# Optimization experiments

Measured on AMD Instinct MI355X. Metric: run time of the kernel, lower is better.

The kernel has to match this reference:

```python
import jax, jax.numpy as jnp
import numpy as np

NEG = -1e9  # masked-out (non-edge) additive bias


def _attn_head(seq, bias_mat, W1, a1, b1, a2, b2, W2, bW):
    # seq: [B,N,F]; W1: [F,H]; a1,a2: [H]; W2: [H,K]
    fts = jnp.einsum('bnf,fh->bnh', seq, W1)            # Conv1D(out_sz,1,no bias)
    f1 = jnp.einsum('bnh,h->bn', fts, a1) + b1          # Conv1D(1,1)
    f2 = jnp.einsum('bnh,h->bn', fts, a2) + b2          # Conv1D(1,1)
    logits = f1[:, :, None] + f2[:, None, :]            # [B,N,N] additive attention
    coefs = jax.nn.softmax(jax.nn.leaky_relu(logits, 0.2) + bias_mat, axis=-1)
    vals = jnp.einsum('bnm,bmh->bnh', coefs, fts)       # weighted aggregation
    return jnp.einsum('bnh,hk->bnk', vals, W2) + bW     # bias_add_layer1 (Dense)


def setup_inputs() -> dict:
    B, N, F, H, NH, C = 1, 4096, 512, 64, 8, 40
    key = jax.random.key(0)
    ks = jax.random.split(key, 12)
    seq = jax.random.normal(ks[0], (B, N, F), dtype=jnp.float32)
    adj = jax.random.bernoulli(ks[1], 0.01, (B, N, N)) | jnp.eye(N, dtype=bool)[None]
    bias_mat = jnp.where(adj, 0.0, NEG).astype(jnp.float32)
    s = 0.05
    # 8 stacked first-layer heads (out_sz=H)
    W1 = jax.random.normal(ks[2], (NH, F, H), dtype=jnp.float32) * s
    a1 = jax.random.normal(ks[3], (NH, H), dtype=jnp.float32) * s
    b1 = jnp.zeros((NH,), jnp.float32)
    a2 = jax.random.normal(ks[4], (NH, H), dtype=jnp.float32) * s
    b2 = jnp.zeros((NH,), jnp.float32)
    W2 = jax.random.normal(ks[5], (NH, H, H), dtype=jnp.float32) * s
    bW = jnp.zeros((NH, H), jnp.float32)
    # single output head (out_sz=nb_classes, identity activation)
    Wo1 = jax.random.normal(ks[6], (NH * H, C), dtype=jnp.float32) * s
    ao1 = jax.random.normal(ks[7], (C,), dtype=jnp.float32) * s
    bo1 = jnp.zeros((), jnp.float32)
    ao2 = jax.random.normal(ks[8], (C,), dtype=jnp.float32) * s
    bo2 = jnp.zeros((), jnp.float32)
    Wo2 = jax.random.normal(ks[9], (C, C), dtype=jnp.float32) * s
    bo = jnp.zeros((C,), jnp.float32)
    return dict(seq=seq, bias_mat=bias_mat, W1=W1, a1=a1, b1=b1, a2=a2, b2=b2,
                W2=W2, bW=bW, Wo1=Wo1, ao1=ao1, bo1=bo1, ao2=ao2, bo2=bo2,
                Wo2=Wo2, bo=bo)


def reference(seq, bias_mat, W1, a1, b1, a2, b2, W2, bW,
              Wo1, ao1, bo1, ao2, bo2, Wo2, bo):
    # first layer: 8 heads with elu activation, vmapped over head params
    heads = jax.vmap(
        lambda w1, v1, c1, v2, c2, w2, bw: jax.nn.elu(
            _attn_head(seq, bias_mat, w1, v1, c1, v2, c2, w2, bw))
    )(W1, a1, b1, a2, b2, W2, bW)                        # [NH,B,N,H]
    NH, B, N, H = heads.shape
    h1 = jnp.moveaxis(heads, 0, 2).reshape(B, N, NH * H)  # concat along features
    # output layer: 1 head, identity activation, averaged over n_heads[-1]=1
    out = _attn_head(h1, bias_mat, Wo1, ao1, bo1, ao2, bo2, Wo2, bo)
    return out / 1.0
```

## Files before the change

kernel.cpp:

```cpp
#include <hip/hip_runtime.h>
#include <cstdint>
#include <cstddef>

#define NN 4096
#define FDIM 512
#define HDIM 64
#define NHEAD 8
#define CDIM 40
#define MAXD 256

typedef __attribute__((ext_vector_type(8))) short bf16x8;
typedef __attribute__((ext_vector_type(16))) float f32x16;

__device__ __forceinline__ float wave_max64(float v) {
  for (int o = 32; o; o >>= 1) v = fmaxf(v, __shfl_xor(v, o));
  return v;
}
__device__ __forceinline__ float wave_sum64(float v) {
  for (int o = 32; o; o >>= 1) v += __shfl_xor(v, o);
  return v;
}
__device__ __forceinline__ float readlane_f(float v, int sl) {
  return __uint_as_float((unsigned)__builtin_amdgcn_readlane((int)__float_as_uint(v), sl));
}
__device__ __forceinline__ int readlane_i(int v, int sl) {
  return __builtin_amdgcn_readlane(v, sl);
}
__device__ __forceinline__ unsigned short f2bf(float x) {
  unsigned u = __float_as_uint(x);
  return (unsigned short)((u + 0x7fffu + ((u >> 16) & 1u)) >> 16);
}
__device__ __forceinline__ float bf2f(unsigned short b) {
  return __uint_as_float(((unsigned)b) << 16);
}

__global__ __launch_bounds__(256) void k_prep(
    const float* __restrict__ seq, short* __restrict__ Ahi, short* __restrict__ Alo,
    const float* __restrict__ W1, short* __restrict__ Bhi, short* __restrict__ Blo,
    const float* __restrict__ W2, short* __restrict__ W2thi, short* __restrict__ W2tlo,
    const float* __restrict__ Wo1, short* __restrict__ Wo1thi, short* __restrict__ Wo1tlo) {
  __shared__ float T[64][65];
  int bx = blockIdx.x, tid = threadIdx.x;
  if (bx < 1024) {
    size_t off = (size_t)bx * 2048 + (size_t)tid * 8;
    float4 v0 = *(const float4*)(seq + off);
    float4 v1 = *(const float4*)(seq + off + 4);
    unsigned short h0 = f2bf(v0.x), h1 = f2bf(v0.y), h2 = f2bf(v0.z), h3 = f2bf(v0.w);
    unsigned short h4 = f2bf(v1.x), h5 = f2bf(v1.y), h6 = f2bf(v1.z), h7 = f2bf(v1.w);
    *(uint4*)(Ahi + off) = make_uint4(
        (unsigned)h0 | ((unsigned)h1 << 16), (unsigned)h2 | ((unsigned)h3 << 16),
        (unsigned)h4 | ((unsigned)h5 << 16), (unsigned)h6 | ((unsigned)h7 << 16));
    unsigned short l0 = f2bf(v0.x - bf2f(h0)), l1 = f2bf(v0.y - bf2f(h1));
    unsigned short l2 = f2bf(v0.z - bf2f(h2)), l3 = f2bf(v0.w - bf2f(h3));
    unsigned short l4 = f2bf(v1.x - bf2f(h4)), l5 = f2bf(v1.y - bf2f(h5));
    unsigned short l6 = f2bf(v1.z - bf2f(h6)), l7 = f2bf(v1.w - bf2f(h7));
    *(uint4*)(Alo + off) = make_uint4(
        (unsigned)l0 | ((unsigned)l1 << 16), (unsigned)l2 | ((unsigned)l3 << 16),
        (unsigned)l4 | ((unsigned)l5 << 16), (unsigned)l6 | ((unsigned)l7 << 16));
    return;
  }
  bx -= 1024;
  if (bx < 64) {
    int h = bx >> 3, kb = bx & 7;
    const float* src = W1 + ((size_t)h * FDIM + kb * 64) * HDIM;
#pragma unroll
    for (int q = 0; q < 4; ++q) {
      int fi = q * 256 + tid, kk = fi >> 4, n4 = fi & 15;
      float4 v = *(const float4*)(src + (size_t)kk * HDIM + n4 * 4);
      T[n4 * 4 + 0][kk] = v.x; T[n4 * 4 + 1][kk] = v.y;
      T[n4 * 4 + 2][kk] = v.z; T[n4 * 4 + 3][kk] = v.w;
    }
    __syncthreads();
#pragma unroll
    for (int q = 0; q < 4; ++q) {
      int fi = q * 256 + tid, n = fi >> 4, k4 = fi & 15;
      float a = T[n][k4 * 4], b = T[n][k4 * 4 + 1];
      float c = T[n][k4 * 4 + 2], d = T[n][k4 * 4 + 3];
      size_t o = ((size_t)h * 64 + n) * FDIM + kb * 64 + k4 * 4;
      unsigned short ha = f2bf(a), hb = f2bf(b), hc = f2bf(c), hd = f2bf(d);
      *(short4*)(Bhi + o) = make_short4((short)ha, (short)hb, (short)hc, (short)hd);
      *(short4*)(Blo + o) = make_short4((short)f2bf(a - bf2f(ha)), (short)f2bf(b - bf2f(hb)),
                                        (short)f2bf(c - bf2f(hc)), (short)f2bf(d - bf2f(hd)));
    }
    return;
  }
  bx -= 64;
  if (bx < 8) {
    int h = bx;
    const float* src = W2 + (size_t)h * HDIM * HDIM;
#pragma unroll
    for (int q = 0; q < 4; ++q) {
      int fi = q * 256 + tid, kk = fi >> 4, n4 = fi & 15;
      float4 v = *(const float4*)(src + (size_t)kk * HDIM + n4 * 4);
      T[n4 * 4 + 0][kk] = v.x; T[n4 * 4 + 1][kk] = v.y;
      T[n4 * 4 + 2][kk] = v.z; T[n4 * 4 + 3][kk] = v.w;
    }
    __syncthreads();
#pragma unroll
    for (int q = 0; q < 4; ++q) {
      int fi = q * 256 + tid, n = fi >> 4, k4 = fi & 15;
      float a = T[n][k4 * 4], b = T[n][k4 * 4 + 1];
      float c = T[n][k4 * 4 + 2], d = T[n][k4 * 4 + 3];
      size_t o = (size_t)h * 4096 + (size_t)n * 64 + k4 * 4;
      unsigned short ha = f2bf(a), hb = f2bf(b), hc = f2bf(c), hd = f2bf(d);
      *(short4*)(W2thi + o) = make_short4((short)ha, (short)hb, (short)hc, (short)hd);
      *(short4*)(W2tlo + o) = make_short4((short)f2bf(a - bf2f(ha)), (short)f2bf(b - bf2f(hb)),
                                          (short)f2bf(c - bf2f(hc)), (short)f2bf(d - bf2f(hd)));
    }
    return;
  }
  bx -= 8;
  {
#pragma unroll
    for (int q = 0; q < 16; ++q) {
      int idx = q * 256 + tid;
      int n = bx * 8 + (idx >> 9), k = idx & 511;
      float v = (n < CDIM) ? Wo1[(size_t)k * CDIM + n] : 0.f;
      unsigned short hv = f2bf(v);
      Wo1thi[(size_t)n * FDIM + k] = (short)hv;
      Wo1tlo[(size_t)n * FDIM + k] = (short)f2bf(v - bf2f(hv));
    }
  }
}

__global__ __launch_bounds__(256) void k_gemm(
    const short* __restrict__ Ahi, const short* __restrict__ Alo,
    const short* __restrict__ Bhi, const short* __restrict__ Blo,
    const float* __restrict__ a1, const float* __restrict__ b1,
    const float* __restrict__ a2, const float* __restrict__ b2,
    short* __restrict__ FTSb, float* __restrict__ F1t, float* __restrict__ F2t,
    const float* __restrict__ bias, int* __restrict__ nbr, int* __restrict__ cnt) {
  __shared__ short AH[4][64][16], AL[4][64][16];
  __shared__ short BH[4][128][16], BL[4][128][16];
  __shared__ int wtot[4];
  const int bx = blockIdx.x;
  const int tid = threadIdx.x, lane = tid & 63, w = tid >> 6;

  if (bx >= 256) {
    int row = bx - 256;
    int wv = w;
    const float4* r = (const float4*)(bias + (size_t)row * NN);
    unsigned mask = 0;
#pragma unroll
    for (int i = 0; i < 4; ++i) {
      float4 v = r[tid * 4 + i];
      mask |= (unsigned)((v.x == 0.f ? 1 : 0) | (v.y == 0.f ? 2 : 0) |
                         (v.z == 0.f ? 4 : 0) | (v.w == 0.f ? 8 : 0)) << (i * 4);
    }
    int c = __popc(mask);
    int pre = c;
#pragma unroll
    for (int o = 1; o < 64; o <<= 1) {
      int u = __shfl_up(pre, o);
      if (lane >= o) pre += u;
    }
    if (lane == 63) wtot[wv] = pre;
    __syncthreads();
    int woff = 0;
#pragma unroll
    for (int ww = 0; ww < 4; ++ww)
      if (ww < wv) woff += wtot[ww];
    int excl = woff + pre - c;
    int* outp = nbr + (size_t)row * MAXD;
    int col0 = tid * 16, k = 0;
#pragma unroll
    for (int i = 0; i < 16; ++i) {
      if ((mask >> i) & 1) {
        int p = excl + k;
        if (p < MAXD) outp[p] = col0 + i;
        ++k;
      }
    }
    if (tid == 0) {
      int total = wtot[0] + wtot[1] + wtot[2] + wtot[3];
      cnt[row] = total < MAXD ? total : MAXD;
    }
    return;
  }

  const int mtile = bx & 63, npair = bx >> 6;
  const int wm = w >> 1, wn = w & 1;
  const int ml = lane & 31, g = lane >> 5, g8 = g * 8;

  f32x16 acc0, acc1;
#pragma unroll
  for (int r = 0; r < 16; ++r) { acc0[r] = 0.f; acc1[r] = 0.f; }

  const short* Abh = Ahi + (((size_t)mtile * 64) << 9);
  const short* Abl = Alo + (((size_t)mtile * 64) << 9);
  const short* Bbh = Bhi + (((size_t)npair * 128) << 9);
  const short* Bbl = Blo + (((size_t)npair * 128) << 9);

  const int tn = tid >> 3, k8 = tid & 7;
  const int ks = k8 >> 1, ko = (k8 & 1) * 8;
  const size_t so = ((size_t)tn << 9) + (size_t)k8 * 8;

  int4 rah0, rah1, ral0, ral1, rbh0, rbh1, rbh2, rbh3, rbl0, rbl1, rbl2, rbl3;
  {
    rah0 = *(const int4*)(Abh + so);              ral0 = *(const int4*)(Abl + so);
    rah1 = *(const int4*)(Abh + so + (32 << 9));  ral1 = *(const int4*)(Abl + so + (32 << 9));
    rbh0 = *(const int4*)(Bbh + so);              rbl0 = *(const int4*)(Bbl + so);
    rbh1 = *(const int4*)(Bbh + so + (32 << 9));  rbl1 = *(const int4*)(Bbl + so + (32 << 9));
    rbh2 = *(const int4*)(Bbh + so + (64 << 9));  rbl2 = *(const int4*)(Bbl + so + (64 << 9));
    rbh3 = *(const int4*)(Bbh + so + (96 << 9));  rbl3 = *(const int4*)(Bbl + so + (96 << 9));
  }

  const int NCH = FDIM / 64;
  for (int c = 0; c < NCH; ++c) {
    *(int4*)&AH[ks][tn][ko] = rah0;       *(int4*)&AL[ks][tn][ko] = ral0;
    *(int4*)&AH[ks][32 + tn][ko] = rah1;  *(int4*)&AL[ks][32 + tn][ko] = ral1;
    *(int4*)&BH[ks][tn][ko] = rbh0;       *(int4*)&BL[ks][tn][ko] = rbl0;
    *(int4*)&BH[ks][32 + tn][ko] = rbh1;  *(int4*)&BL[ks][32 + tn][ko] = rbl1;
    *(int4*)&BH[ks][64 + tn][ko] = rbh2;  *(int4*)&BL[ks][64 + tn][ko] = rbl2;
    *(int4*)&BH[ks][96 + tn][ko] = rbh3;  *(int4*)&BL[ks][96 + tn][ko] = rbl3;
    __syncthreads();
    if (c + 1 < NCH) {
      size_t o = so + (size_t)(c + 1) * 64;
      rah0 = *(const int4*)(Abh + o);              ral0 = *(const int4*)(Abl + o);
      rah1 = *(const int4*)(Abh + o + (32 << 9));  ral1 = *(const int4*)(Abl + o + (32 << 9));
      rbh0 = *(const int4*)(Bbh + o);              rbl0 = *(const int4*)(Bbl + o);
      rbh1 = *(const int4*)(Bbh + o + (32 << 9));  rbl1 = *(const int4*)(Bbl + o + (32 << 9));
      rbh2 = *(const int4*)(Bbh + o + (64 << 9));  rbl2 = *(const int4*)(Bbl + o + (64 << 9));
      rbh3 = *(const int4*)(Bbh + o + (96 << 9));  rbl3 = *(const int4*)(Bbl + o + (96 << 9));
    }
#pragma unroll
    for (int t = 0; t < 4; ++t) {
      bf16x8 ah = *(const bf16x8*)&AH[t][wm * 32 + ml][g8];
      bf16x8 al = *(const bf16x8*)&AL[t][wm * 32 + ml][g8];
      bf16x8 bh0 = *(const bf16x8*)&BH[t][wn * 64 + ml][g8];
      bf16x8 bl0 = *(const bf16x8*)&BL[t][wn * 64 + ml][g8];
      acc0 = __builtin_amdgcn_mfma_f32_32x32x16_bf16(ah, bh0, acc0, 0, 0, 0);
      acc0 = __builtin_amdgcn_mfma_f32_32x32x16_bf16(al, bh0, acc0, 0, 0, 0);
      acc0 = __builtin_amdgcn_mfma_f32_32x32x16_bf16(ah, bl0, acc0, 0, 0, 0);
      bf16x8 bh1 = *(const bf16x8*)&BH[t][wn * 64 + 32 + ml][g8];
      bf16x8 bl1 = *(const bf16x8*)&BL[t][wn * 64 + 32 + ml][g8];
      acc1 = __builtin_amdgcn_mfma_f32_32x32x16_bf16(ah, bh1, acc1, 0, 0, 0);
      acc1 = __builtin_amdgcn_mfma_f32_32x32x16_bf16(al, bh1, acc1, 0, 0, 0);
      acc1 = __builtin_amdgcn_mfma_f32_32x32x16_bf16(ah, bl1, acc1, 0, 0, 0);
    }
    __syncthreads();
  }

  const int h = npair * 2 + wn;
  const float a1lo = a1[h * 64 + ml], a1hi = a1[h * 64 + 32 + ml];
  const float a2lo = a2[h * 64 + ml], a2hi = a2[h * 64 + 32 + ml];
  const float b1h = b1[h], b2h = b2[h];
  const int row0 = mtile * 64 + wm * 32 + 4 * g;
  const int col0 = npair * 128 + wn * 64 + ml;
#pragma unroll
  for (int r = 0; r < 16; ++r) {
    int row = row0 + (r & 3) + 8 * (r >> 2);
    FTSb[(size_t)row * FDIM + col0] = (short)f2bf(acc0[r]);
    FTSb[(size_t)row * FDIM + col0 + 32] = (short)f2bf(acc1[r]);
    float p1 = acc0[r] * a1lo + acc1[r] * a1hi;
    float p2 = acc0[r] * a2lo + acc1[r] * a2hi;
#pragma unroll
    for (int o = 1; o < 32; o <<= 1) {
      p1 += __shfl_xor(p1, o);
      p2 += __shfl_xor(p2, o);
    }
    if (ml == 0) {
      F1t[(size_t)row * 8 + h] = p1 + b1h;
      F2t[(size_t)row * 8 + h] = p2 + b2h;
    }
  }
}

__global__ __launch_bounds__(256) void k_agg1(
    const short* __restrict__ FTSb, const float* __restrict__ F1t,
    const float* __restrict__ F2t, const int* __restrict__ nbr,
    const int* __restrict__ cnt, short* __restrict__ VALShi,
    short* __restrict__ VALSlo) {
  __shared__ float plds[4][MAXD][4];
  int wv = threadIdx.x >> 6, lane = threadIdx.x & 63;
  int gw = blockIdx.x * 4 + wv;
  int i = gw >> 1, hg = gw & 1;
  int deg = cnt[i];
  const int* nb = nbr + (size_t)i * MAXD;
  float4 f1v = *(const float4*)(F1t + (size_t)i * 8 + hg * 4);

  float4 p4[4];
  int jreg[4];
  float mx = -1e30f, my = -1e30f, mz = -1e30f, mw = -1e30f;
#pragma unroll
  for (int r = 0; r < 4; ++r) {
    int t = r * 64 + lane;
    jreg[r] = 0;
    p4[r] = make_float4(-1e30f, -1e30f, -1e30f, -1e30f);
    if (t < deg) {
      int j = nb[t];
      jreg[r] = j;
      float4 f2v = *(const float4*)(F2t + (size_t)j * 8 + hg * 4);
      float4 x;
      x.x = f1v.x + f2v.x; x.x = x.x >= 0.f ? x.x : 0.2f * x.x;
      x.y = f1v.y + f2v.y; x.y = x.y >= 0.f ? x.y : 0.2f * x.y;
      x.z = f1v.z + f2v.z; x.z = x.z >= 0.f ? x.z : 0.2f * x.z;
      x.w = f1v.w + f2v.w; x.w = x.w >= 0.f ? x.w : 0.2f * x.w;
      p4[r] = x;
      mx = fmaxf(mx, x.x); my = fmaxf(my, x.y);
      mz = fmaxf(mz, x.z); mw = fmaxf(mw, x.w);
    }
  }
  mx = wave_max64(mx); my = wave_max64(my);
  mz = wave_max64(mz); mw = wave_max64(mw);
  float sx = 0.f, sy = 0.f, sz = 0.f, sw = 0.f;
#pragma unroll
  for (int r = 0; r < 4; ++r) {
    int t = r * 64 + lane;
    float4 e = make_float4(0.f, 0.f, 0.f, 0.f);
    if (t < deg) {
      e.x = __expf(p4[r].x - mx); e.y = __expf(p4[r].y - my);
      e.z = __expf(p4[r].z - mz); e.w = __expf(p4[r].w - mw);
    }
    p4[r] = e;
    sx += e.x; sy += e.y; sz += e.z; sw += e.w;
    *(float4*)&plds[wv][r * 64 + lane][0] = e;
  }
  sx = wave_sum64(sx); sy = wave_sum64(sy);
  sz = wave_sum64(sz); sw = wave_sum64(sw);

  int q = lane >> 4;
  float invh = (q < 2) ? (q == 0 ? 1.f / sx : 1.f / sy)
                       : (q == 2 ? 1.f / sz : 1.f / sw);

  float4 accA = make_float4(0.f, 0.f, 0.f, 0.f);
  float4 accB = make_float4(0.f, 0.f, 0.f, 0.f);
  float4 accC = make_float4(0.f, 0.f, 0.f, 0.f);
  float4 accD = make_float4(0.f, 0.f, 0.f, 0.f);
  const short* Fb = FTSb + hg * 256;
#pragma unroll
  for (int r = 0; r < 4; ++r) {
    int base = r * 64;
    if (base >= deg) break;
    int lim = deg - base;
    lim = lim < 64 ? lim : 64;
    int sl = 0;
    for (; sl + 4 <= lim; sl += 4) {
      int j0 = readlane_i(jreg[r], sl);
      int j1 = readlane_i(jreg[r], sl + 1);
      int j2 = readlane_i(jreg[r], sl + 2);
      int j3 = readlane_i(jreg[r], sl + 3);
      float wA = plds[wv][base + sl][q];
      float wB = plds[wv][base + sl + 1][q];
      float wC = plds[wv][base + sl + 2][q];
      float wD = plds[wv][base + sl + 3][q];
      short4 s0 = *(const short4*)(Fb + (size_t)j0 * FDIM + lane * 4);
      short4 s1 = *(const short4*)(Fb + (size_t)j1 * FDIM + lane * 4);
      short4 s2 = *(const short4*)(Fb + (size_t)j2 * FDIM + lane * 4);
      short4 s3 = *(const short4*)(Fb + (size_t)j3 * FDIM + lane * 4);
      accA.x += wA * bf2f((unsigned short)s0.x); accA.y += wA * bf2f((unsigned short)s0.y);
      accA.z += wA * bf2f((unsigned short)s0.z); accA.w += wA * bf2f((unsigned short)s0.w);
      accB.x += wB * bf2f((unsigned short)s1.x); accB.y += wB * bf2f((unsigned short)s1.y);
      accB.z += wB * bf2f((unsigned short)s1.z); accB.w += wB * bf2f((unsigned short)s1.w);
      accC.x += wC * bf2f((unsigned short)s2.x); accC.y += wC * bf2f((unsigned short)s2.y);
      accC.z += wC * bf2f((unsigned short)s2.z); accC.w += wC * bf2f((unsigned short)s2.w);
      accD.x += wD * bf2f((unsigned short)s3.x); accD.y += wD * bf2f((unsigned short)s3.y);
      accD.z += wD * bf2f((unsigned short)s3.z); accD.w += wD * bf2f((unsigned short)s3.w);
    }
    for (; sl < lim; ++sl) {
      int j0 = readlane_i(jreg[r], sl);
      float wA = plds[wv][base + sl][q];
      short4 s0 = *(const short4*)(Fb + (size_t)j0 * FDIM + lane * 4);
      accA.x += wA * bf2f((unsigned short)s0.x); accA.y += wA * bf2f((unsigned short)s0.y);
      accA.z += wA * bf2f((unsigned short)s0.z); accA.w += wA * bf2f((unsigned short)s0.w);
    }
  }
  float vx = (accA.x + accB.x + accC.x + accD.x) * invh;
  float vy = (accA.y + accB.y + accC.y + accD.y) * invh;
  float vz = (accA.z + accB.z + accC.z + accD.z) * invh;
  float vw = (accA.w + accB.w + accC.w + accD.w) * invh;
  unsigned short hx = f2bf(vx), hy = f2bf(vy), hz = f2bf(vz), hw = f2bf(vw);
  size_t o = (size_t)i * FDIM + hg * 256 + lane * 4;
  *(short4*)(VALShi + o) = make_short4((short)hx, (short)hy, (short)hz, (short)hw);
  *(short4*)(VALSlo + o) = make_short4(
      (short)f2bf(vx - bf2f(hx)), (short)f2bf(vy - bf2f(hy)),
      (short)f2bf(vz - bf2f(hz)), (short)f2bf(vw - bf2f(hw)));
}

__global__ __launch_bounds__(256) void k_tail(
    const short* __restrict__ VALShi, const short* __restrict__ VALSlo,
    const short* __restrict__ W2thi, const short* __restrict__ W2tlo,
    const float* __restrict__ bW,
    const short* __restrict__ Wo1thi, const short* __restrict__ Wo1tlo,
    const float* __restrict__ ao1, const float* __restrict__ bo1s,
    const float* __restrict__ ao2, const float* __restrict__ bo2s,
    float* __restrict__ FTS2, float* __restrict__ F1O, float* __restrict__ F2O) {
  __shared__ short AH[4][64][16], AL[4][64][16];
  __shared__ short BH[4][64][16], BL[4][64][16];
  __shared__ short CH[4][64][16], CL[4][64][16];
  __shared__ short DH[4][64][16], DL[4][64][16];
  __shared__ float p1buf[2][64], p2buf[2][64];
  const int i0 = blockIdx.x * 64;
  const int tid = threadIdx.x, lane = tid & 63, w = tid >> 6;
  const int wm = w >> 1, wn = w & 1;
  const int ml = lane & 31, g = lane >> 5, g8 = g * 8;
  const int tn = tid >> 2, k8 = tid & 3;
  const int colw = wn * 32 + ml;
  const int rowl0 = wm * 32 + 4 * g;

  f32x16 acc2;
#pragma unroll
  for (int r = 0; r < 16; ++r) acc2[r] = 0.f;

  for (int h = 0; h < NHEAD; ++h) {
    {
      const short* pa = VALShi + ((size_t)(i0 + tn) << 9) + h * 64 + k8 * 16;
      const short* pl = VALSlo + ((size_t)(i0 + tn) << 9) + h * 64 + k8 * 16;
      *(int4*)&AH[k8][tn][0] = *(const int4*)pa;
      *(int4*)&AH[k8][tn][8] = *(const int4*)(pa + 8);
      *(int4*)&AL[k8][tn][0] = *(const int4*)pl;
      *(int4*)&AL[k8][tn][8] = *(const int4*)(pl + 8);
      const short* pb  = W2thi + (size_t)h * 4096 + tn * 64 + k8 * 16;
      const short* pbl = W2tlo + (size_t)h * 4096 + tn * 64 + k8 * 16;
      *(int4*)&BH[k8][tn][0] = *(const int4*)pb;
      *(int4*)&BH[k8][tn][8] = *(const int4*)(pb + 8);
      *(int4*)&BL[k8][tn][0] = *(const int4*)pbl;
      *(int4*)&BL[k8][tn][8] = *(const int4*)(pbl + 8);
      const short* pd  = Wo1thi + (size_t)tn * FDIM + h * 64 + k8 * 16;
      const short* pdl = Wo1tlo + (size_t)tn * FDIM + h * 64 + k8 * 16;
      *(int4*)&DH[k8][tn][0] = *(const int4*)pd;
      *(int4*)&DH[k8][tn][8] = *(const int4*)(pd + 8);
      *(int4*)&DL[k8][tn][0] = *(const int4*)pdl;
      *(int4*)&DL[k8][tn][8] = *(const int4*)(pdl + 8);
    }
    __syncthreads();
    f32x16 accw;
#pragma unroll
    for (int r = 0; r < 16; ++r) accw[r] = 0.f;
#pragma unroll
    for (int t = 0; t < 4; ++t) {
      bf16x8 ah = *(const bf16x8*)&AH[t][wm * 32 + ml][g8];
      bf16x8 al = *(const bf16x8*)&AL[t][wm * 32 + ml][g8];
      bf16x8 bh = *(const bf16x8*)&BH[t][wn * 32 + ml][g8];
      bf16x8 bl = *(const bf16x8*)&BL[t][wn * 32 + ml][g8];
      accw = __builtin_amdgcn_mfma_f32_32x32x16_bf16(ah, bh, accw, 0, 0, 0);
      accw = __builtin_amdgcn_mfma_f32_32x32x16_bf16(al, bh, accw, 0, 0, 0);
      accw = __builtin_amdgcn_mfma_f32_32x32x16_bf16(ah, bl, accw, 0, 0, 0);
    }
    const float bwv = bW[h * 64 + colw];
    const int ts = colw >> 4, ss = colw & 15;
#pragma unroll
    for (int r = 0; r < 16; ++r) {
      int rl = rowl0 + (r & 3) + 8 * (r >> 2);
      float v = accw[r] + bwv;
      v = v > 0.f ? v : __expf(v) - 1.f;
      unsigned short hv = f2bf(v);
      CH[ts][rl][ss] = (short)hv;
      CL[ts][rl][ss] = (short)f2bf(v - bf2f(hv));
    }
    __syncthreads();
#pragma unroll
    for (int t = 0; t < 4; ++t) {
      bf16x8 ah = *(const bf16x8*)&CH[t][wm * 32 + ml][g8];
      bf16x8 al = *(const bf16x8*)&CL[t][wm * 32 + ml][g8];
      bf16x8 bh = *(const bf16x8*)&DH[t][wn * 32 + ml][g8];
      bf16x8 bl = *(const bf16x8*)&DL[t][wn * 32 + ml][g8];
      acc2 = __builtin_amdgcn_mfma_f32_32x32x16_bf16(ah, bh, acc2, 0, 0, 0);
      acc2 = __builtin_amdgcn_mfma_f32_32x32x16_bf16(al, bh, acc2, 0, 0, 0);
      acc2 = __builtin_amdgcn_mfma_f32_32x32x16_bf16(ah, bl, acc2, 0, 0, 0);
    }
    __syncthreads();
  }

  const bool act = colw < CDIM;
  const float aov1 = act ? ao1[colw] : 0.f;
  const float aov2 = act ? ao2[colw] : 0.f;
#pragma unroll
  for (int r = 0; r < 16; ++r) {
    int rl = rowl0 + (r & 3) + 8 * (r >> 2);
    float v = acc2[r];
    if (act) FTS2[(size_t)(i0 + rl) * CDIM + colw] = v;
    float p1 = v * aov1, p2 = v * aov2;
#pragma unroll
    for (int o = 1; o < 32; o <<= 1) {
      p1 += __shfl_xor(p1, o);
      p2 += __shfl_xor(p2, o);
    }
    if (ml == 0) {
      p1buf[wn][rl] = p1;
      p2buf[wn][rl] = p2;
    }
  }
  __syncthreads();
  if (tid < 64) {
    F1O[i0 + tid] = p1buf[0][tid] + p1buf[1][tid] + bo1s[0];
    F2O[i0 + tid] = p2buf[0][tid] + p2buf[1][tid] + bo2s[0];
  }
}

__global__ __launch_bounds__(256) void k_agg2(
    const float* __restrict__ FTS2, const float* __restrict__ F1O,
    const float* __restrict__ F2O, const int* __restrict__ nbr,
    const int* __restrict__ cnt, const float* __restrict__ Wo2,
    const float* __restrict__ bo, float* __restrict__ out) {
  int i = blockIdx.x * 4 + (threadIdx.x >> 6);
  int lane = threadIdx.x & 63;
  int deg = cnt[i];
  const int* nb = nbr + (size_t)i * MAXD;
  float f1i = F1O[i];

  int jreg[4];
  float p[4];
  float m = -1e30f;
#pragma unroll
  for (int r = 0; r < 4; ++r) { jreg[r] = 0; p[r] = -1e30f; }
#pragma unroll
  for (int r = 0; r < 4; ++r) {
    int t = r * 64 + lane;
    if (t < deg) {
      int j = nb[t];
      jreg[r] = j;
      float x = f1i + F2O[j];
      x = x >= 0.f ? x : 0.2f * x;
      p[r] = x;
      m = fmaxf(m, x);
    }
  }
  m = wave_max64(m);
  float s = 0.f;
#pragma unroll
  for (int r = 0; r < 4; ++r) {
    int t = r * 64 + lane;
    float e = (t < deg) ? __expf(p[r] - m) : 0.f;
    p[r] = e;
    s += e;
  }
  s = wave_sum64(s);

  const bool act = lane < CDIM;
  float accA = 0.f, accB = 0.f, accC = 0.f, accD = 0.f;
#pragma unroll
  for (int r = 0; r < 4; ++r) {
    int base = r * 64;
    if (base >= deg) break;
    int lim = deg - base;
    lim = lim < 64 ? lim : 64;
    int sl = 0;
    for (; sl + 4 <= lim; sl += 4) {
      float w0 = readlane_f(p[r], sl);
      float w1 = readlane_f(p[r], sl + 1);
      float w2 = readlane_f(p[r], sl + 2);
      float w3 = readlane_f(p[r], sl + 3);
      int j0 = readlane_i(jreg[r], sl);
      int j1 = readlane_i(jreg[r], sl + 1);
      int j2 = readlane_i(jreg[r], sl + 2);
      int j3 = readlane_i(jreg[r], sl + 3);
      float f0 = act ? FTS2[(size_t)j0 * CDIM + lane] : 0.f;
      float f1 = act ? FTS2[(size_t)j1 * CDIM + lane] : 0.f;
      float f2 = act ? FTS2[(size_t)j2 * CDIM + lane] : 0.f;
      float f3 = act ? FTS2[(size_t)j3 * CDIM + lane] : 0.f;
      accA += w0 * f0;
      accB += w1 * f1;
      accC += w2 * f2;
      accD += w3 * f3;
    }
    for (; sl < lim; ++sl) {
      float w0 = readlane_f(p[r], sl);
      int j0 = readlane_i(jreg[r], sl);
      float f0 = act ? FTS2[(size_t)j0 * CDIM + lane] : 0.f;
      accA += w0 * f0;
    }
  }
  float v = (accA + accB + accC + accD) / s;

  float o = act ? bo[lane] : 0.f;
  for (int kk = 0; kk < CDIM; ++kk) {
    float w = readlane_f(v, kk);
    float b = act ? Wo2[kk * CDIM + lane] : 0.f;
    o += w * b;
  }
  if (act) out[(size_t)i * CDIM + lane] = o;
}

extern "C" void kernel_launch(void* const* d_in, const int* in_sizes, int n_in,
                              void* d_out, int out_size, void* d_ws, size_t ws_size,
                              hipStream_t stream) {
  const float* seq  = (const float*)d_in[0];
  const float* bias = (const float*)d_in[1];
  const float* W1   = (const float*)d_in[2];
  const float* a1   = (const float*)d_in[3];
  const float* b1   = (const float*)d_in[4];
  const float* a2   = (const float*)d_in[5];
  const float* b2   = (const float*)d_in[6];
  const float* W2   = (const float*)d_in[7];
  const float* bW   = (const float*)d_in[8];
  const float* Wo1  = (const float*)d_in[9];
  const float* ao1  = (const float*)d_in[10];
  const float* bo1  = (const float*)d_in[11];
  const float* ao2  = (const float*)d_in[12];
  const float* bo2  = (const float*)d_in[13];
  const float* Wo2  = (const float*)d_in[14];
  const float* bo   = (const float*)d_in[15];
  float* out = (float*)d_out;

  float* ws    = (float*)d_ws;
  float* F1t   = ws;
  float* F2t   = F1t  + (size_t)NN * NHEAD;
  float* FTS2  = F2t  + (size_t)NN * NHEAD;
  float* F1O   = FTS2 + (size_t)NN * CDIM;
  float* F2O   = F1O  + NN;
  short* FTSb  = (short*)(F2O + NN);
  short* Ahi   = FTSb + (size_t)NN * FDIM;
  short* Alo   = Ahi + (size_t)NN * FDIM;
  short* Bhi   = Alo + (size_t)NN * FDIM;
  short* Blo   = Bhi + (size_t)NHEAD * HDIM * FDIM;
  short* VALShi= Blo + (size_t)NHEAD * HDIM * FDIM;
  short* VALSlo= VALShi + (size_t)NN * FDIM;
  short* W2thi = VALSlo + (size_t)NN * FDIM;
  short* W2tlo = W2thi + (size_t)NHEAD * HDIM * HDIM;
  short* Wo1thi= W2tlo + (size_t)NHEAD * HDIM * HDIM;
  short* Wo1tlo= Wo1thi + (size_t)64 * FDIM;
  int*   nbr   = (int*)(Wo1tlo + (size_t)64 * FDIM);
  int*   cnt   = nbr + (size_t)NN * MAXD;

  k_prep<<<1024 + 64 + 8 + 8, 256, 0, stream>>>(
      seq, Ahi, Alo, W1, Bhi, Blo, W2, W2thi, W2tlo, Wo1, Wo1thi, Wo1tlo);
  k_gemm<<<256 + NN, 256, 0, stream>>>(
      Ahi, Alo, Bhi, Blo, a1, b1, a2, b2, FTSb, F1t, F2t, bias, nbr, cnt);
  k_agg1<<<NN * 2 / 4, 256, 0, stream>>>(FTSb, F1t, F2t, nbr, cnt, VALShi, VALSlo);
  k_tail<<<NN / 64, 256, 0, stream>>>(VALShi, VALSlo, W2thi, W2tlo, bW,
                                      Wo1thi, Wo1tlo, ao1, bo1, ao2, bo2,
                                      FTS2, F1O, F2O);
  k_agg2<<<NN / 4, 256, 0, stream>>>(FTS2, F1O, F2O, nbr, cnt, Wo2, bo, out);
}
```

Baseline: 87.30 us.

## Fuse seq bf16 split into GEMM loads and widen agg1 to all heads per wave

The GEMM kernel now reads fp32 seq directly and splits it into bf16 hi/lo in registers before the LDS store. This removes the separate prep pass that wrote Ahi/Alo and the later re-read of those arrays. The first aggregation kernel now has one wave handle all 8 heads of a node instead of two waves with 4 heads each. That halves the neighbor-index and F2 gathers and uses 16-byte feature loads per lane, in exchange for more registers per wave and repeated conversion work in each GEMM tile that shares the same A rows.

After: 85.00 us. 1.03x faster.

```diff
diff --git a/kernel.cpp b/kernel.cpp
--- a/kernel.cpp
+++ b/kernel.cpp
@@ -33,33 +33,32 @@
 __device__ __forceinline__ float bf2f(unsigned short b) {
   return __uint_as_float(((unsigned)b) << 16);
 }
+__device__ __forceinline__ float lo16f(int u) { return __int_as_float(u << 16); }
+__device__ __forceinline__ float hi16f(int u) { return __int_as_float(u & 0xffff0000); }
+__device__ __forceinline__ void cvt8(const float4& a, const float4& b,
+                                     int4& hi, int4& lo) {
+  unsigned short h0 = f2bf(a.x), h1 = f2bf(a.y), h2 = f2bf(a.z), h3 = f2bf(a.w);
+  unsigned short h4 = f2bf(b.x), h5 = f2bf(b.y), h6 = f2bf(b.z), h7 = f2bf(b.w);
+  hi = make_int4((int)((unsigned)h0 | ((unsigned)h1 << 16)),
+                 (int)((unsigned)h2 | ((unsigned)h3 << 16)),
+                 (int)((unsigned)h4 | ((unsigned)h5 << 16)),
+                 (int)((unsigned)h6 | ((unsigned)h7 << 16)));
+  unsigned short l0 = f2bf(a.x - bf2f(h0)), l1 = f2bf(a.y - bf2f(h1));
+  unsigned short l2 = f2bf(a.z - bf2f(h2)), l3 = f2bf(a.w - bf2f(h3));
+  unsigned short l4 = f2bf(b.x - bf2f(h4)), l5 = f2bf(b.y - bf2f(h5));
+  unsigned short l6 = f2bf(b.z - bf2f(h6)), l7 = f2bf(b.w - bf2f(h7));
+  lo = make_int4((int)((unsigned)l0 | ((unsigned)l1 << 16)),
+                 (int)((unsigned)l2 | ((unsigned)l3 << 16)),
+                 (int)((unsigned)l4 | ((unsigned)l5 << 16)),
+                 (int)((unsigned)l6 | ((unsigned)l7 << 16)));
+}
 
 __global__ __launch_bounds__(256) void k_prep(
-    const float* __restrict__ seq, short* __restrict__ Ahi, short* __restrict__ Alo,
     const float* __restrict__ W1, short* __restrict__ Bhi, short* __restrict__ Blo,
     const float* __restrict__ W2, short* __restrict__ W2thi, short* __restrict__ W2tlo,
     const float* __restrict__ Wo1, short* __restrict__ Wo1thi, short* __restrict__ Wo1tlo) {
   __shared__ float T[64][65];
   int bx = blockIdx.x, tid = threadIdx.x;
-  if (bx < 1024) {
-    size_t off = (size_t)bx * 2048 + (size_t)tid * 8;
-    float4 v0 = *(const float4*)(seq + off);
-    float4 v1 = *(const float4*)(seq + off + 4);
-    unsigned short h0 = f2bf(v0.x), h1 = f2bf(v0.y), h2 = f2bf(v0.z), h3 = f2bf(v0.w);
-    unsigned short h4 = f2bf(v1.x), h5 = f2bf(v1.y), h6 = f2bf(v1.z), h7 = f2bf(v1.w);
-    *(uint4*)(Ahi + off) = make_uint4(
-        (unsigned)h0 | ((unsigned)h1 << 16), (unsigned)h2 | ((unsigned)h3 << 16),
-        (unsigned)h4 | ((unsigned)h5 << 16), (unsigned)h6 | ((unsigned)h7 << 16));
-    unsigned short l0 = f2bf(v0.x - bf2f(h0)), l1 = f2bf(v0.y - bf2f(h1));
-    unsigned short l2 = f2bf(v0.z - bf2f(h2)), l3 = f2bf(v0.w - bf2f(h3));
-    unsigned short l4 = f2bf(v1.x - bf2f(h4)), l5 = f2bf(v1.y - bf2f(h5));
-    unsigned short l6 = f2bf(v1.z - bf2f(h6)), l7 = f2bf(v1.w - bf2f(h7));
-    *(uint4*)(Alo + off) = make_uint4(
-        (unsigned)l0 | ((unsigned)l1 << 16), (unsigned)l2 | ((unsigned)l3 << 16),
-        (unsigned)l4 | ((unsigned)l5 << 16), (unsigned)l6 | ((unsigned)l7 << 16));
-    return;
-  }
-  bx -= 1024;
   if (bx < 64) {
     int h = bx >> 3, kb = bx & 7;
     const float* src = W1 + ((size_t)h * FDIM + kb * 64) * HDIM;
@@ -124,7 +123,7 @@
 }
 
 __global__ __launch_bounds__(256) void k_gemm(
-    const short* __restrict__ Ahi, const short* __restrict__ Alo,
+    const float* __restrict__ seq,
     const short* __restrict__ Bhi, const short* __restrict__ Blo,
     const float* __restrict__ a1, const float* __restrict__ b1,
     const float* __restrict__ a2, const float* __restrict__ b2,
@@ -186,19 +185,20 @@
 #pragma unroll
   for (int r = 0; r < 16; ++r) { acc0[r] = 0.f; acc1[r] = 0.f; }
 
-  const short* Abh = Ahi + (((size_t)mtile * 64) << 9);
-  const short* Abl = Alo + (((size_t)mtile * 64) << 9);
   const short* Bbh = Bhi + (((size_t)npair * 128) << 9);
   const short* Bbl = Blo + (((size_t)npair * 128) << 9);
 
   const int tn = tid >> 3, k8 = tid & 7;
   const int ks = k8 >> 1, ko = (k8 & 1) * 8;
   const size_t so = ((size_t)tn << 9) + (size_t)k8 * 8;
-
-  int4 rah0, rah1, ral0, ral1, rbh0, rbh1, rbh2, rbh3, rbl0, rbl1, rbl2, rbl3;
+  const float* As0 = seq + (((size_t)(mtile * 64 + tn)) << 9) + k8 * 8;
+  const float* As1 = As0 + ((size_t)32 << 9);
+
+  float4 fa0a, fa0b, fa1a, fa1b;
+  int4 rbh0, rbh1, rbh2, rbh3, rbl0, rbl1, rbl2, rbl3;
   {
-    rah0 = *(const int4*)(Abh + so);              ral0 = *(const int4*)(Abl + so);
-    rah1 = *(const int4*)(Abh + so + (32 << 9));  ral1 = *(const int4*)(Abl + so + (32 << 9));
+    fa0a = *(const float4*)(As0);      fa0b = *(const float4*)(As0 + 4);
+    fa1a = *(const float4*)(As1);      fa1b = *(const float4*)(As1 + 4);
     rbh0 = *(const int4*)(Bbh + so);              rbl0 = *(const int4*)(Bbl + so);
     rbh1 = *(const int4*)(Bbh + so + (32 << 9));  rbl1 = *(const int4*)(Bbl + so + (32 << 9));
     rbh2 = *(const int4*)(Bbh + so + (64 << 9));  rbl2 = *(const int4*)(Bbl + so + (64 << 9));
@@ -207,8 +207,13 @@
 
   const int NCH = FDIM / 64;
   for (int c = 0; c < NCH; ++c) {
-    *(int4*)&AH[ks][tn][ko] = rah0;       *(int4*)&AL[ks][tn][ko] = ral0;
-    *(int4*)&AH[ks][32 + tn][ko] = rah1;  *(int4*)&AL[ks][32 + tn][ko] = ral1;
+    {
+      int4 hi0, lo0, hi1, lo1;
+      cvt8(fa0a, fa0b, hi0, lo0);
+      cvt8(fa1a, fa1b, hi1, lo1);
+      *(int4*)&AH[ks][tn][ko] = hi0;       *(int4*)&AL[ks][tn][ko] = lo0;
+      *(int4*)&AH[ks][32 + tn][ko] = hi1;  *(int4*)&AL[ks][32 + tn][ko] = lo1;
+    }
     *(int4*)&BH[ks][tn][ko] = rbh0;       *(int4*)&BL[ks][tn][ko] = rbl0;
     *(int4*)&BH[ks][32 + tn][ko] = rbh1;  *(int4*)&BL[ks][32 + tn][ko] = rbl1;
     *(int4*)&BH[ks][64 + tn][ko] = rbh2;  *(int4*)&BL[ks][64 + tn][ko] = rbl2;
@@ -216,8 +221,10 @@
     __syncthreads();
     if (c + 1 < NCH) {
       size_t o = so + (size_t)(c + 1) * 64;
-      rah0 = *(const int4*)(Abh + o);              ral0 = *(const int4*)(Abl + o);
-      rah1 = *(const int4*)(Abh + o + (32 << 9));  ral1 = *(const int4*)(Abl + o + (32 << 9));
+      const float* a0 = As0 + (size_t)(c + 1) * 64;
+      const float* a1p = As1 + (size_t)(c + 1) * 64;
+      fa0a = *(const float4*)(a0);      fa0b = *(const float4*)(a0 + 4);
+      fa1a = *(const float4*)(a1p);     fa1b = *(const float4*)(a1p + 4);
       rbh0 = *(const int4*)(Bbh + o);              rbl0 = *(const int4*)(Bbl + o);
       rbh1 = *(const int4*)(Bbh + o + (32 << 9));  rbl1 = *(const int4*)(Bbl + o + (32 << 9));
       rbh2 = *(const int4*)(Bbh + o + (64 << 9));  rbl2 = *(const int4*)(Bbl + o + (64 << 9));
@@ -271,63 +278,74 @@
     const float* __restrict__ F2t, const int* __restrict__ nbr,
     const int* __restrict__ cnt, short* __restrict__ VALShi,
     short* __restrict__ VALSlo) {
-  __shared__ float plds[4][MAXD][4];
+  __shared__ float plds[4][MAXD][8];
   int wv = threadIdx.x >> 6, lane = threadIdx.x & 63;
-  int gw = blockIdx.x * 4 + wv;
-  int i = gw >> 1, hg = gw & 1;
+  int i = blockIdx.x * 4 + wv;
   int deg = cnt[i];
   const int* nb = nbr + (size_t)i * MAXD;
-  float4 f1v = *(const float4*)(F1t + (size_t)i * 8 + hg * 4);
-
-  float4 p4[4];
+  float4 f1a = *(const float4*)(F1t + (size_t)i * 8);
+  float4 f1b = *(const float4*)(F1t + (size_t)i * 8 + 4);
+
+  float4 pa[4], pb[4];
   int jreg[4];
-  float mx = -1e30f, my = -1e30f, mz = -1e30f, mw = -1e30f;
+  float m0 = -1e30f, m1 = -1e30f, m2 = -1e30f, m3 = -1e30f;
+  float m4 = -1e30f, m5 = -1e30f, m6 = -1e30f, m7 = -1e30f;
 #pragma unroll
   for (int r = 0; r < 4; ++r) {
     int t = r * 64 + lane;
     jreg[r] = 0;
-    p4[r] = make_float4(-1e30f, -1e30f, -1e30f, -1e30f);
+    pa[r] = make_float4(-1e30f, -1e30f, -1e30f, -1e30f);
+    pb[r] = pa[r];
     if (t < deg) {
       int j = nb[t];
       jreg[r] = j;
-      float4 f2v = *(const float4*)(F2t + (size_t)j * 8 + hg * 4);
-      float4 x;
-      x.x = f1v.x + f2v.x; x.x = x.x >= 0.f ? x.x : 0.2f * x.x;
-      x.y = f1v.y + f2v.y; x.y = x.y >= 0.f ? x.y : 0.2f * x.y;
-      x.z = f1v.z + f2v.z; x.z = x.z >= 0.f ? x.z : 0.2f * x.z;
-      x.w = f1v.w + f2v.w; x.w = x.w >= 0.f ? x.w : 0.2f * x.w;
-      p4[r] = x;
-      mx = fmaxf(mx, x.x); my = fmaxf(my, x.y);
-      mz = fmaxf(mz, x.z); mw = fmaxf(mw, x.w);
-    }
-  }
-  mx = wave_max64(mx); my = wave_max64(my);
-  mz = wave_max64(mz); mw = wave_max64(mw);
-  float sx = 0.f, sy = 0.f, sz = 0.f, sw = 0.f;
+      float4 f2a = *(const float4*)(F2t + (size_t)j * 8);
+      float4 f2b = *(const float4*)(F2t + (size_t)j * 8 + 4);
+      float4 xa, xb;
+      xa.x = f1a.x + f2a.x; xa.x = xa.x >= 0.f ? xa.x : 0.2f * xa.x;
+      xa.y = f1a.y + f2a.y; xa.y = xa.y >= 0.f ? xa.y : 0.2f * xa.y;
+      xa.z = f1a.z + f2a.z; xa.z = xa.z >= 0.f ? xa.z : 0.2f * xa.z;
+      xa.w = f1a.w + f2a.w; xa.w = xa.w >= 0.f ? xa.w : 0.2f * xa.w;
+      xb.x = f1b.x + f2b.x; xb.x = xb.x >= 0.f ? xb.x : 0.2f * xb.x;
+      xb.y = f1b.y + f2b.y; xb.y = xb.y >= 0.f ? xb.y : 0.2f * xb.y;
+      xb.z = f1b.z + f2b.z; xb.z = xb.z >= 0.f ? xb.z : 0.2f * xb.z;
+      xb.w = f1b.w + f2b.w; xb.w = xb.w >= 0.f ? xb.w : 0.2f * xb.w;
+      pa[r] = xa; pb[r] = xb;
+      m0 = fmaxf(m0, xa.x); m1 = fmaxf(m1, xa.y);
+      m2 = fmaxf(m2, xa.z); m3 = fmaxf(m3, xa.w);
+      m4 = fmaxf(m4, xb.x); m5 = fmaxf(m5, xb.y);
+      m6 = fmaxf(m6, xb.z); m7 = fmaxf(m7, xb.w);
+    }
+  }
+  m0 = wave_max64(m0); m1 = wave_max64(m1); m2 = wave_max64(m2); m3 = wave_max64(m3);
+  m4 = wave_max64(m4); m5 = wave_max64(m5); m6 = wave_max64(m6); m7 = wave_max64(m7);
+  float s0 = 0.f, s1 = 0.f, s2 = 0.f, s3 = 0.f, s4 = 0.f, s5 = 0.f, s6 = 0.f, s7 = 0.f;
 #pragma unroll
   for (int r = 0; r < 4; ++r) {
     int t = r * 64 + lane;
-    float4 e = make_float4(0.f, 0.f, 0.f, 0.f);
+    float4 ea = make_float4(0.f, 0.f, 0.f, 0.f), eb = ea;
     if (t < deg) {
-      e.x = __expf(p4[r].x - mx); e.y = __expf(p4[r].y - my);
-      e.z = __expf(p4[r].z - mz); e.w = __expf(p4[r].w - mw);
-    }
-    p4[r] = e;
-    sx += e.x; sy += e.y; sz += e.z; sw += e.w;
-    *(float4*)&plds[wv][r * 64 + lane][0] = e;
-  }
-  sx = wave_sum64(sx); sy = wave_sum64(sy);
-  sz = wave_sum64(sz); sw = wave_sum64(sw);
-
-  int q = lane >> 4;
-  float invh = (q < 2) ? (q == 0 ? 1.f / sx : 1.f / sy)
-                       : (q == 2 ? 1.f / sz : 1.f / sw);
-
-  float4 accA = make_float4(0.f, 0.f, 0.f, 0.f);
-  float4 accB = make_float4(0.f, 0.f, 0.f, 0.f);
-  float4 accC = make_float4(0.f, 0.f, 0.f, 0.f);
-  float4 accD = make_float4(0.f, 0.f, 0.f, 0.f);
-  const short* Fb = FTSb + hg * 256;
+      ea.x = __expf(pa[r].x - m0); ea.y = __expf(pa[r].y - m1);
+      ea.z = __expf(pa[r].z - m2); ea.w = __expf(pa[r].w - m3);
+      eb.x = __expf(pb[r].x - m4); eb.y = __expf(pb[r].y - m5);
+      eb.z = __expf(pb[r].z - m6); eb.w = __expf(pb[r].w - m7);
+      *(float4*)&plds[wv][t][0] = ea;
+      *(float4*)&plds[wv][t][4] = eb;
+    }
+    s0 += ea.x; s1 += ea.y; s2 += ea.z; s3 += ea.w;
+    s4 += eb.x; s5 += eb.y; s6 += eb.z; s7 += eb.w;
+  }
+  s0 = wave_sum64(s0); s1 = wave_sum64(s1); s2 = wave_sum64(s2); s3 = wave_sum64(s3);
+  s4 = wave_sum64(s4); s5 = wave_sum64(s5); s6 = wave_sum64(s6); s7 = wave_sum64(s7);
+
+  const int q = lane >> 3;
+  float sq = (q < 4) ? (q < 2 ? (q == 0 ? s0 : s1) : (q == 2 ? s2 : s3))
+                     : (q < 6 ? (q == 4 ? s4 : s5) : (q == 6 ? s6 : s7));
+  float inv = 1.f / sq;
+
+  float4 aA = make_float4(0.f, 0.f, 0.f, 0.f), bA = aA;
+  float4 aB = aA, bB = aA, aC = aA, bC = aA, aD = aA, bD = aA;
+  const size_t lo8 = (size_t)lane * 8;
 #pragma unroll
   for (int r = 0; r < 4; ++r) {
     int base = r * 64;
@@ -340,41 +358,61 @@
       int j1 = readlane_i(jreg[r], sl + 1);
       int j2 = readlane_i(jreg[r], sl + 2);
       int j3 = readlane_i(jreg[r], sl + 3);
-      float wA = plds[wv][base + sl][q];
-      float wB = plds[wv][base + sl + 1][q];
-      float wC = plds[wv][base + sl + 2][q];
-      float wD = plds[wv][base + sl + 3][q];
-      short4 s0 = *(const short4*)(Fb + (size_t)j0 * FDIM + lane * 4);
-      short4 s1 = *(const short4*)(Fb + (size_t)j1 * FDIM + lane * 4);
-      short4 s2 = *(const short4*)(Fb + (size_t)j2 * FDIM + lane * 4);
-      short4 s3 = *(const short4*)(Fb + (size_t)j3 * FDIM + lane * 4);
-      accA.x += wA * bf2f((unsigned short)s0.x); accA.y += wA * bf2f((unsigned short)s0.y);
-      accA.z += wA * bf2f((unsigned short)s0.z); accA.w += wA * bf2f((unsigned short)s0.w);
-      accB.x += wB * bf2f((unsigned short)s1.x); accB.y += wB * bf2f((unsigned short)s1.y);
-      accB.z += wB * bf2f((unsigned short)s1.z); accB.w += wB * bf2f((unsigned short)s1.w);
-      accC.x += wC * bf2f((unsigned short)s2.x); accC.y += wC * bf2f((unsigned short)s2.y);
-      accC.z += wC * bf2f((unsigned short)s2.z); accC.w += wC * bf2f((unsigned short)s2.w);
-      accD.x += wD * bf2f((unsigned short)s3.x); accD.y += wD * bf2f((unsigned short)s3.y);
-      accD.z += wD * bf2f((unsigned short)s3.z); accD.w += wD * bf2f((unsigned short)s3.w);
+      float w0 = plds[wv][base + sl][q];
+      float w1 = plds[wv][base + sl + 1][q];
+      float w2 = plds[wv][base + sl + 2][q];
+      float w3 = plds[wv][base + sl + 3][q];
+      int4 g0 = *(const int4*)(FTSb + (size_t)j0 * FDIM + lo8);
+      int4 g1 = *(const int4*)(FTSb + (size_t)j1 * FDIM + lo8);
+      int4 g2 = *(const int4*)(FTSb + (size_t)j2 * FDIM + lo8);
+      int4 g3 = *(const int4*)(FTSb + (size_t)j3 * FDIM + lo8);
+      aA.x += w0 * lo16f(g0.x); aA.y += w0 * hi16f(g0.x);
+      aA.z += w0 * lo16f(g0.y); aA.w += w0 * hi16f(g0.y);
+      bA.x += w0 * lo16f(g0.z); bA.y += w0 * hi16f(g0.z);
+      bA.z += w0 * lo16f(g0.w); bA.w += w0 * hi16f(g0.w);
+      aB.x += w1 * lo16f(g1.x); aB.y += w1 * hi16f(g1.x);
+      aB.z += w1 * lo16f(g1.y); aB.w += w1 * hi16f(g1.y);
+      bB.x += w1 * lo16f(g1.z); bB.y += w1 * hi16f(g1.z);
+      bB.z += w1 * lo16f(g1.w); bB.w += w1 * hi16f(g1.w);
+      aC.x += w2 * lo16f(g2.x); aC.y += w2 * hi16f(g2.x);
+      aC.z += w2 * lo16f(g2.y); aC.w += w2 * hi16f(g2.y);
+      bC.x += w2 * lo16f(g2.z); bC.y += w2 * hi16f(g2.z);
+      bC.z += w2 * lo16f(g2.w); bC.w += w2 * hi16f(g2.w);
+      aD.x += w3 * lo16f(g3.x); aD.y += w3 * hi16f(g3.x);
+      aD.z += w3 * lo16f(g3.y); aD.w += w3 * hi16f(g3.y);
+      bD.x += w3 * lo16f(g3.z); bD.y += w3 * hi16f(g3.z);
+      bD.z += w3 * lo16f(g3.w); bD.w += w3 * hi16f(g3.w);
     }
     for (; sl < lim; ++sl) {
       int j0 = readlane_i(jreg[r], sl);
-      float wA = plds[wv][base + sl][q];
-      short4 s0 = *(const short4*)(Fb + (size_t)j0 * FDIM + lane * 4);
-      accA.x += wA * bf2f((unsigned short)s0.x); accA.y += wA * bf2f((unsigned short)s0.y);
-      accA.z += wA * bf2f((unsigned short)s0.z); accA.w += wA * bf2f((unsigned short)s0.w);
-    }
-  }
-  float vx = (accA.x + accB.x + accC.x + accD.x) * invh;
-  float vy = (accA.y + accB.y + accC.y + accD.y) * invh;
-  float vz = (accA.z + accB.z + accC.z + accD.z) * invh;
-  float vw = (accA.w + accB.w + accC.w + accD.w) * invh;
-  unsigned short hx = f2bf(vx), hy = f2bf(vy), hz = f2bf(vz), hw = f2bf(vw);
-  size_t o = (size_t)i * FDIM + hg * 256 + lane * 4;
-  *(short4*)(VALShi + o) = make_short4((short)hx, (short)hy, (short)hz, (short)hw);
-  *(short4*)(VALSlo + o) = make_short4(
-      (short)f2bf(vx - bf2f(hx)), (short)f2bf(vy - bf2f(hy)),
-      (short)f2bf(vz - bf2f(hz)), (short)f2bf(vw - bf2f(hw)));
+      float w0 = plds[wv][base + sl][q];
+      int4 g0 = *(const int4*)(FTSb + (size_t)j0 * FDIM + lo8);
+      aA.x += w0 * lo16f(g0.x); aA.y += w0 * hi16f(g0.x);
+      aA.z += w0 * lo16f(g0.y); aA.w += w0 * hi16f(g0.y);
+      bA.x += w0 * lo16f(g0.z); bA.y += w0 * hi16f(g0.z);
+      bA.z += w0 * lo16f(g0.w); bA.w += w0 * hi16f(g0.w);
+    }
+  }
+  float v0 = (aA.x + aB.x + aC.x + aD.x) * inv;
+  float v1 = (aA.y + aB.y + aC.y + aD.y) * inv;
+  float v2 = (aA.z + aB.z + aC.z + aD.z) * inv;
+  float v3 = (aA.w + aB.w + aC.w + aD.w) * inv;
+  float v4 = (bA.x + bB.x + bC.x + bD.x) * inv;
+  float v5 = (bA.y + bB.y + bC.y + bD.y) * inv;
+  float v6 = (bA.z + bB.z + bC.z + bD.z) * inv;
+  float v7 = (bA.w + bB.w + bC.w + bD.w) * inv;
+  unsigned short h0 = f2bf(v0), h1 = f2bf(v1), h2 = f2bf(v2), h3 = f2bf(v3);
+  unsigned short h4 = f2bf(v4), h5 = f2bf(v5), h6 = f2bf(v6), h7 = f2bf(v7);
+  *(int4*)(VALShi + (size_t)i * FDIM + lo8) = make_int4(
+      (int)((unsigned)h0 | ((unsigned)h1 << 16)), (int)((unsigned)h2 | ((unsigned)h3 << 16)),
+      (int)((unsigned)h4 | ((unsigned)h5 << 16)), (int)((unsigned)h6 | ((unsigned)h7 << 16)));
+  unsigned short l0 = f2bf(v0 - bf2f(h0)), l1 = f2bf(v1 - bf2f(h1));
+  unsigned short l2 = f2bf(v2 - bf2f(h2)), l3 = f2bf(v3 - bf2f(h3));
+  unsigned short l4 = f2bf(v4 - bf2f(h4)), l5 = f2bf(v5 - bf2f(h5));
+  unsigned short l6 = f2bf(v6 - bf2f(h6)), l7 = f2bf(v7 - bf2f(h7));
+  *(int4*)(VALSlo + (size_t)i * FDIM + lo8) = make_int4(
+      (int)((unsigned)l0 | ((unsigned)l1 << 16)), (int)((unsigned)l2 | ((unsigned)l3 << 16)),
+      (int)((unsigned)l4 | ((unsigned)l5 << 16)), (int)((unsigned)l6 | ((unsigned)l7 << 16)));
 }
 
 __global__ __launch_bounds__(256) void k_tail(
@@ -600,9 +638,7 @@
   float* F1O   = FTS2 + (size_t)NN * CDIM;
   float* F2O   = F1O  + NN;
   short* FTSb  = (short*)(F2O + NN);
-  short* Ahi   = FTSb + (size_t)NN * FDIM;
-  short* Alo   = Ahi + (size_t)NN * FDIM;
-  short* Bhi   = Alo + (size_t)NN * FDIM;
+  short* Bhi   = FTSb + (size_t)NN * FDIM;
   short* Blo   = Bhi + (size_t)NHEAD * HDIM * FDIM;
   short* VALShi= Blo + (size_t)NHEAD * HDIM * FDIM;
   short* VALSlo= VALShi + (size_t)NN * FDIM;
@@ -613,11 +649,11 @@
   int*   nbr   = (int*)(Wo1tlo + (size_t)64 * FDIM);
   int*   cnt   = nbr + (size_t)NN * MAXD;
 
-  k_prep<<<1024 + 64 + 8 + 8, 256, 0, stream>>>(
-      seq, Ahi, Alo, W1, Bhi, Blo, W2, W2thi, W2tlo, Wo1, Wo1thi, Wo1tlo);
+  k_prep<<<64 + 8 + 8, 256, 0, stream>>>(
+      W1, Bhi, Blo, W2, W2thi, W2tlo, Wo1, Wo1thi, Wo1tlo);
   k_gemm<<<256 + NN, 256, 0, stream>>>(
-      Ahi, Alo, Bhi, Blo, a1, b1, a2, b2, FTSb, F1t, F2t, bias, nbr, cnt);
-  k_agg1<<<NN * 2 / 4, 256, 0, stream>>>(FTSb, F1t, F2t, nbr, cnt, VALShi, VALSlo);
+      seq, Bhi, Blo, a1, b1, a2, b2, FTSb, F1t, F2t, bias, nbr, cnt);
+  k_agg1<<<NN / 4, 256, 0, stream>>>(FTSb, F1t, F2t, nbr, cnt, VALShi, VALSlo);
   k_tail<<<NN / 64, 256, 0, stream>>>(VALShi, VALSlo, W2thi, W2tlo, bW,
                                       Wo1thi, Wo1tlo, ao1, bo1, ao2, bo2,
                                       FTS2, F1O, F2O);
```
